# Kernel optimization log

Hardware: AMD Instinct MI355X
Metric: run time of the kernel (lower is better)

The kernel has to match this reference:

```python
import jax, jax.numpy as jnp
import numpy as np

FP8_MAX = 448.0  # float8_e4m3 max finite value


def setup_inputs() -> dict:
    key = jax.random.key(0)
    k1, k2, k3, k4, k5 = jax.random.split(key, 5)
    B, S, IN, OUT = 8, 2048, 2048, 2048
    x = jax.random.normal(k1, (B, S, IN), dtype=jnp.float32)
    weight = jax.random.normal(k2, (OUT, IN), dtype=jnp.float32) * 0.02
    bias = jax.random.normal(k3, (OUT,), dtype=jnp.float32)
    # per-tensor scales, kept positive and away from zero
    scale_in = jax.random.uniform(k4, (1,), dtype=jnp.float32) * 0.09 + 0.01
    scale_w = jax.random.uniform(k5, (1,), dtype=jnp.float32) * 0.09 + 0.01
    return {"x": x, "weight": weight, "bias": bias,
            "scale_in": scale_in, "scale_w": scale_w}


def _fp8_quantize(x, scale):
    # divide by scale, saturate to fp8 range, cast to fp8 e4m3
    q = jnp.clip(x / scale, -FP8_MAX, FP8_MAX)
    return q.astype(jnp.float8_e4m3fn)


def reference(x, weight, bias, scale_in, scale_w):
    # quantize input and weight to fp8 (per-tensor scales)
    xq = _fp8_quantize(x, scale_in)            # [B,S,IN] fp8
    wq = _fp8_quantize(weight, scale_w)        # [OUT,IN] fp8
    # scaled matmul: accumulate in fp32, dequant with scale_a*scale_b, emit fp16
    acc = jnp.einsum('bsk,nk->bsn', xq.astype(jnp.float32), wq.astype(jnp.float32))
    out = (acc * (scale_in[0] * scale_w[0])).astype(jnp.float16)
    out = out + bias.astype(jnp.float16)       # trailing bias add at fp16
    return out
```

## Files before the change

kernel.cpp:

```cpp
#include <hip/hip_runtime.h>
#include <hip/hip_fp16.h>
#include <stdint.h>

#define MDIM 16384
#define NDIM 2048
#define KDIM 2048

typedef __attribute__((ext_vector_type(4))) float f32x4;
typedef __attribute__((ext_vector_type(4))) int   i32x4;
typedef __attribute__((ext_vector_type(8))) int   i32x8;

__device__ __forceinline__ unsigned f32_to_e4m3(float x) {
    float q = fminf(448.f, fmaxf(-448.f, x));
    unsigned ub = __float_as_uint(q);
    unsigned sgn = (ub >> 24) & 0x80u;
    float aq = fabsf(q);
    int E = (int)((__float_as_uint(aq) >> 23) & 0xff) - 127;
    if (E < -6) E = -6;
    float rq = __uint_as_float((unsigned)(130 - E) << 23);
    int m = (int)rintf(aq * rq);
    if (m == 16) { m = 8; E += 1; }
    unsigned bits;
    if (m < 8) bits = sgn | (unsigned)m;
    else       bits = sgn | ((unsigned)(E + 7) << 3) | (unsigned)(m - 8);
    return bits;
}

__device__ __forceinline__ void quant_span(const float* __restrict__ x,
                                           uint8_t* __restrict__ q, float sc,
                                           unsigned i0, unsigned stride,
                                           unsigned n16) {
    for (unsigned i = i0; i < n16; i += stride) {
        const float4* xp = (const float4*)(x + (size_t)i * 16);
        uint32_t w[4];
#pragma unroll
        for (int j = 0; j < 4; ++j) {
            float4 v = xp[j];
            w[j] = f32_to_e4m3(v.x / sc) | (f32_to_e4m3(v.y / sc) << 8) |
                   (f32_to_e4m3(v.z / sc) << 16) | (f32_to_e4m3(v.w / sc) << 24);
        }
        ((uint4*)q)[i] = make_uint4(w[0], w[1], w[2], w[3]);
    }
}

__global__ void quant_both_kernel(const float* __restrict__ x,
                                  uint8_t* __restrict__ xq,
                                  const float* __restrict__ w,
                                  uint8_t* __restrict__ wq,
                                  const float* __restrict__ s_in,
                                  const float* __restrict__ s_w) {
    if (blockIdx.x < 2048) {
        unsigned i0 = blockIdx.x * 256 + threadIdx.x;
        quant_span(x, xq, s_in[0], i0, 2048 * 256,
                   (unsigned)((size_t)MDIM * KDIM / 16));
    } else {
        unsigned i0 = (blockIdx.x - 2048) * 256 + threadIdx.x;
        quant_span(w, wq, s_w[0], i0, 256 * 256,
                   (unsigned)((size_t)NDIM * KDIM / 16));
    }
}

#define BM 256
#define BN 256
#define BKB 128
#define NKT (KDIM / BKB)

__device__ __forceinline__ void gload_lds16(const uint8_t* g, uint8_t* l) {
    __builtin_amdgcn_global_load_lds(
        (const __attribute__((address_space(1))) void*)g,
        (__attribute__((address_space(3))) void*)l, 16, 0, 0);
}

__device__ __forceinline__ void barrier_raw() {
    asm volatile("" ::: "memory");
    __builtin_amdgcn_s_barrier();
    asm volatile("" ::: "memory");
}

__global__ __launch_bounds__(512) void gemm_fp8_kernel(
    const uint8_t* __restrict__ Aq, const uint8_t* __restrict__ Bq,
    const float* __restrict__ bias, const float* __restrict__ s_in,
    const float* __restrict__ s_w, float* __restrict__ out) {

    extern __shared__ uint8_t lds[];

    int nwg = gridDim.x;
    int cpx = nwg >> 3;
    int bid = blockIdx.x;
    int swz = (bid & 7) * cpx + (bid >> 3);
    int tm = swz >> 3;
    int tn = swz & 7;
    int row0 = tm * BM;
    int col0 = tn * BN;

    int tid  = threadIdx.x;
    int lane = tid & 63;
    int wid  = tid >> 6;
    int wr = wid >> 2, wc = wid & 3;
    int r15 = lane & 15;
    int g   = lane >> 4;

    int perm0 = ((2 * g + r15) & 7) << 4;
    int perm1 = ((2 * g + 1 + r15) & 7) << 4;

    int up0 = tid, up1 = 512 + tid;
    int ur0 = up0 >> 3, uc0 = ((up0 & 7) - (ur0 & 7)) & 7;
    int ur1 = up1 >> 3, uc1 = ((up1 & 7) - (ur1 & 7)) & 7;

    const uint8_t* Asrc = Aq + (size_t)row0 * KDIM;
    const uint8_t* Bsrc = Bq + (size_t)col0 * KDIM;

#define STAGE_U(MAT, H, KT)                                                   \
    {                                                                         \
        uint8_t* dst_ = &lds[(((unsigned)(KT) & 1) << 16) + (MAT) * 32768 +   \
                             (H) * 16384];                                    \
        const uint8_t* src_ = (MAT) ? Bsrc : Asrc;                            \
        gload_lds16(src_ + (size_t)((H) * 128 + ur0) * KDIM +                 \
                        (size_t)(KT) * BKB + uc0 * 16,                        \
                    dst_ + up0 * 16);                                         \
        gload_lds16(src_ + (size_t)((H) * 128 + ur1) * KDIM +                 \
                        (size_t)(KT) * BKB + uc1 * 16,                        \
                    dst_ + up1 * 16);                                         \
    }

    f32x4 acc[8][4];
#pragma unroll
    for (int m = 0; m < 8; ++m)
#pragma unroll
        for (int n = 0; n < 4; ++n)
            acc[m][n] = (f32x4){0.f, 0.f, 0.f, 0.f};

    i32x8 af[4], bf[4];

    int aRow0 = wr * 128 + r15;
    int bRow0 = (wc >> 1) * 128 + (wc & 1) * 64 + r15;

#define LOAD_AF(bo, MH)                                                       \
    _Pragma("unroll")                                                         \
    for (int m_ = 0; m_ < 4; ++m_) {                                          \
        const uint8_t* rp = lds + (bo) + (aRow0 + (MH) * 64 + m_ * 16) * 128; \
        i32x4 lo = *(const i32x4*)(rp + perm0);                               \
        i32x4 hi = *(const i32x4*)(rp + perm1);                               \
        _Pragma("unroll")                                                     \
        for (int q_ = 0; q_ < 4; ++q_) { af[m_][q_] = lo[q_]; af[m_][4 + q_] = hi[q_]; } \
    }

#define LOAD_BF2(bo, NH)                                                      \
    _Pragma("unroll")                                                         \
    for (int n_ = 2 * (NH); n_ < 2 * (NH) + 2; ++n_) {                        \
        const uint8_t* rp = lds + (bo) + 32768 + (bRow0 + n_ * 16) * 128;     \
        i32x4 lo = *(const i32x4*)(rp + perm0);                               \
        i32x4 hi = *(const i32x4*)(rp + perm1);                               \
        _Pragma("unroll")                                                     \
        for (int q_ = 0; q_ < 4; ++q_) { bf[n_][q_] = lo[q_]; bf[n_][4 + q_] = hi[q_]; } \
    }

#define MFMA8(MH, NH)                                                         \
    __builtin_amdgcn_s_setprio(1);                                            \
    _Pragma("unroll")                                                         \
    for (int m_ = 0; m_ < 4; ++m_)                                            \
        _Pragma("unroll")                                                     \
        for (int n_ = 2 * (NH); n_ < 2 * (NH) + 2; ++n_)                      \
            acc[(MH) * 4 + m_][n_] =                                          \
                __builtin_amdgcn_mfma_scale_f32_16x16x128_f8f6f4(             \
                    af[m_], bf[n_], acc[(MH) * 4 + m_][n_],                   \
                    0, 0, 0, 127, 0, 127);                                    \
    __builtin_amdgcn_s_setprio(0);

#define LGKM0 asm volatile("s_waitcnt lgkmcnt(0)" ::: "memory")

    STAGE_U(0, 0, 0); STAGE_U(0, 1, 0); STAGE_U(1, 0, 0); STAGE_U(1, 1, 0);
    STAGE_U(1, 0, 1); STAGE_U(1, 1, 1);
    asm volatile("s_waitcnt vmcnt(4)" ::: "memory");
    barrier_raw();

    for (int t = 0; t < NKT; ++t) {
        const unsigned bo = (unsigned)(t & 1) << 16;
        LOAD_AF(bo, 0);
        LOAD_BF2(bo, 0);
        if (t + 1 < NKT) STAGE_U(0, 0, t + 1);
        barrier_raw(); LGKM0;
        MFMA8(0, 0);
        barrier_raw();
        LOAD_BF2(bo, 1);
        if (t + 1 < NKT) STAGE_U(0, 1, t + 1);
        barrier_raw(); LGKM0;
        MFMA8(0, 1);
        barrier_raw();
        LOAD_AF(bo, 1);
        if (t + 2 < NKT) STAGE_U(1, 0, t + 2);
        barrier_raw(); LGKM0;
        MFMA8(1, 0);
        barrier_raw();
        if (t + 2 < NKT) STAGE_U(1, 1, t + 2);
        barrier_raw(); LGKM0;
        MFMA8(1, 1);
        if (t + 2 < NKT) asm volatile("s_waitcnt vmcnt(4)" ::: "memory");
        else             asm volatile("s_waitcnt vmcnt(0)" ::: "memory");
        barrier_raw();
    }

    float s = s_in[0] * s_w[0];
    float* slab = (float*)lds;
    __half hb[4];
#pragma unroll
    for (int n = 0; n < 4; ++n)
        hb[n] = __float2half(bias[col0 + wc * 64 + n * 16 + r15]);

#pragma unroll
    for (int mh = 0; mh < 2; ++mh) {
#pragma unroll
        for (int n = 0; n < 4; ++n) {
            int colb = wc * 64 + n * 16 + r15;
#pragma unroll
            for (int m = 0; m < 4; ++m) {
                int sr = wr * 64 + m * 16 + g * 4;
#pragma unroll
                for (int r = 0; r < 4; ++r) {
                    __half h = __float2half(acc[mh * 4 + m][n][r] * s);
                    slab[(sr + r) * 256 + colb] = __half2float(__hadd(h, hb[n]));
                }
            }
        }
        barrier_raw();
#pragma unroll
        for (int it = 0; it < 16; ++it) {
            int srow = wid * 16 + it;
            f32x4 vv = *(const f32x4*)&slab[srow * 256 + lane * 4];
            int grow = row0 + (srow >> 6) * 128 + mh * 64 + (srow & 63);
            *(f32x4*)&out[(size_t)grow * NDIM + col0 + lane * 4] = vv;
        }
        barrier_raw();
    }
#undef STAGE_U
#undef LOAD_AF
#undef LOAD_BF2
#undef MFMA8
#undef LGKM0
}

extern "C" void kernel_launch(void* const* d_in, const int* in_sizes, int n_in,
                              void* d_out, int out_size, void* d_ws, size_t ws_size,
                              hipStream_t stream) {
    const float* x      = (const float*)d_in[0];
    const float* weight = (const float*)d_in[1];
    const float* bias   = (const float*)d_in[2];
    const float* s_in   = (const float*)d_in[3];
    const float* s_w    = (const float*)d_in[4];
    float* out          = (float*)d_out;

    uint8_t* xq = (uint8_t*)d_ws;
    uint8_t* wq = (uint8_t*)d_ws + (size_t)MDIM * KDIM;

    quant_both_kernel<<<2304, 256, 0, stream>>>(x, xq, weight, wq, s_in, s_w);

    dim3 grid((MDIM / BM) * (NDIM / BN));
    gemm_fp8_kernel<<<grid, 512, 131072, stream>>>(xq, wq, bias, s_in, s_w, out);
}
```

Baseline: 126.9 us.

## Use 4 waves with 128x128 per-wave tiles and simplified double-buffered K loop

```diff
diff --git a/kernel.cpp b/kernel.cpp
--- a/kernel.cpp
+++ b/kernel.cpp
@@ -77,7 +77,7 @@
     asm volatile("" ::: "memory");
 }
 
-__global__ __launch_bounds__(512) void gemm_fp8_kernel(
+__global__ __launch_bounds__(256, 1) void gemm_fp8_kernel(
     const uint8_t* __restrict__ Aq, const uint8_t* __restrict__ Bq,
     const float* __restrict__ bias, const float* __restrict__ s_in,
     const float* __restrict__ s_w, float* __restrict__ out) {
@@ -96,129 +96,120 @@
     int tid  = threadIdx.x;
     int lane = tid & 63;
     int wid  = tid >> 6;
-    int wr = wid >> 2, wc = wid & 3;
+    int wr = wid >> 1, wc = wid & 1;
     int r15 = lane & 15;
     int g   = lane >> 4;
 
     int perm0 = ((2 * g + r15) & 7) << 4;
     int perm1 = ((2 * g + 1 + r15) & 7) << 4;
 
-    int up0 = tid, up1 = 512 + tid;
-    int ur0 = up0 >> 3, uc0 = ((up0 & 7) - (ur0 & 7)) & 7;
-    int ur1 = up1 >> 3, uc1 = ((up1 & 7) - (ur1 & 7)) & 7;
-
+    int stoff[8], sdst[8];
+#pragma unroll
+    for (int j = 0; j < 8; ++j) {
+        int p = j * 256 + tid;
+        int row = p >> 3;
+        int c = ((p & 7) - (row & 7)) & 7;
+        stoff[j] = row * KDIM + c * 16;
+        sdst[j]  = p * 16;
+    }
     const uint8_t* Asrc = Aq + (size_t)row0 * KDIM;
     const uint8_t* Bsrc = Bq + (size_t)col0 * KDIM;
 
-#define STAGE_U(MAT, H, KT)                                                   \
+#define STAGE(KT)                                                             \
     {                                                                         \
-        uint8_t* dst_ = &lds[(((unsigned)(KT) & 1) << 16) + (MAT) * 32768 +   \
-                             (H) * 16384];                                    \
-        const uint8_t* src_ = (MAT) ? Bsrc : Asrc;                            \
-        gload_lds16(src_ + (size_t)((H) * 128 + ur0) * KDIM +                 \
-                        (size_t)(KT) * BKB + uc0 * 16,                        \
-                    dst_ + up0 * 16);                                         \
-        gload_lds16(src_ + (size_t)((H) * 128 + ur1) * KDIM +                 \
-                        (size_t)(KT) * BKB + uc1 * 16,                        \
-                    dst_ + up1 * 16);                                         \
-    }
-
-    f32x4 acc[8][4];
+        uint8_t* dst_ = &lds[((unsigned)(KT) & 1) << 16];                     \
+        _Pragma("unroll")                                                     \
+        for (int j_ = 0; j_ < 8; ++j_)                                        \
+            gload_lds16(Asrc + stoff[j_] + (size_t)(KT) * BKB, dst_ + sdst[j_]); \
+        _Pragma("unroll")                                                     \
+        for (int j_ = 0; j_ < 8; ++j_)                                        \
+            gload_lds16(Bsrc + stoff[j_] + (size_t)(KT) * BKB,                \
+                        dst_ + 32768 + sdst[j_]);                             \
+    }
+
+    f32x4 acc[8][8];
 #pragma unroll
     for (int m = 0; m < 8; ++m)
 #pragma unroll
-        for (int n = 0; n < 4; ++n)
+        for (int n = 0; n < 8; ++n)
             acc[m][n] = (f32x4){0.f, 0.f, 0.f, 0.f};
 
-    i32x8 af[4], bf[4];
-
+    i32x8 af[8], bf0, bf1;
     int aRow0 = wr * 128 + r15;
-    int bRow0 = (wc >> 1) * 128 + (wc & 1) * 64 + r15;
-
-#define LOAD_AF(bo, MH)                                                       \
+    int bRow0 = wc * 128 + r15;
+
+#define LOAD_AF(bo)                                                           \
     _Pragma("unroll")                                                         \
-    for (int m_ = 0; m_ < 4; ++m_) {                                          \
-        const uint8_t* rp = lds + (bo) + (aRow0 + (MH) * 64 + m_ * 16) * 128; \
+    for (int m_ = 0; m_ < 8; ++m_) {                                          \
+        const uint8_t* rp = lds + (bo) + (aRow0 + m_ * 16) * 128;             \
         i32x4 lo = *(const i32x4*)(rp + perm0);                               \
         i32x4 hi = *(const i32x4*)(rp + perm1);                               \
         _Pragma("unroll")                                                     \
         for (int q_ = 0; q_ < 4; ++q_) { af[m_][q_] = lo[q_]; af[m_][4 + q_] = hi[q_]; } \
     }
 
-#define LOAD_BF2(bo, NH)                                                      \
-    _Pragma("unroll")                                                         \
-    for (int n_ = 2 * (NH); n_ < 2 * (NH) + 2; ++n_) {                        \
-        const uint8_t* rp = lds + (bo) + 32768 + (bRow0 + n_ * 16) * 128;     \
+#define LDBF(DST, bo, N)                                                      \
+    {                                                                         \
+        const uint8_t* rp = lds + (bo) + 32768 + (bRow0 + (N) * 16) * 128;    \
         i32x4 lo = *(const i32x4*)(rp + perm0);                               \
         i32x4 hi = *(const i32x4*)(rp + perm1);                               \
         _Pragma("unroll")                                                     \
-        for (int q_ = 0; q_ < 4; ++q_) { bf[n_][q_] = lo[q_]; bf[n_][4 + q_] = hi[q_]; } \
-    }
-
-#define MFMA8(MH, NH)                                                         \
+        for (int q_ = 0; q_ < 4; ++q_) { DST[q_] = lo[q_]; DST[4 + q_] = hi[q_]; } \
+    }
+
+#define MFMA_COL(BF, N)                                                       \
     __builtin_amdgcn_s_setprio(1);                                            \
     _Pragma("unroll")                                                         \
-    for (int m_ = 0; m_ < 4; ++m_)                                            \
-        _Pragma("unroll")                                                     \
-        for (int n_ = 2 * (NH); n_ < 2 * (NH) + 2; ++n_)                      \
-            acc[(MH) * 4 + m_][n_] =                                          \
-                __builtin_amdgcn_mfma_scale_f32_16x16x128_f8f6f4(             \
-                    af[m_], bf[n_], acc[(MH) * 4 + m_][n_],                   \
-                    0, 0, 0, 127, 0, 127);                                    \
+    for (int m_ = 0; m_ < 8; ++m_)                                            \
+        acc[m_][N] = __builtin_amdgcn_mfma_scale_f32_16x16x128_f8f6f4(        \
+            af[m_], BF, acc[m_][N], 0, 0, 0, 127, 0, 127);                    \
     __builtin_amdgcn_s_setprio(0);
 
-#define LGKM0 asm volatile("s_waitcnt lgkmcnt(0)" ::: "memory")
-
-    STAGE_U(0, 0, 0); STAGE_U(0, 1, 0); STAGE_U(1, 0, 0); STAGE_U(1, 1, 0);
-    STAGE_U(1, 0, 1); STAGE_U(1, 1, 1);
-    asm volatile("s_waitcnt vmcnt(4)" ::: "memory");
-    barrier_raw();
+    STAGE(0);
+    STAGE(1);
 
     for (int t = 0; t < NKT; ++t) {
+        if (t + 1 < NKT) asm volatile("s_waitcnt vmcnt(16)" ::: "memory");
+        else             asm volatile("s_waitcnt vmcnt(0)" ::: "memory");
+        barrier_raw();
         const unsigned bo = (unsigned)(t & 1) << 16;
-        LOAD_AF(bo, 0);
-        LOAD_BF2(bo, 0);
-        if (t + 1 < NKT) STAGE_U(0, 0, t + 1);
-        barrier_raw(); LGKM0;
-        MFMA8(0, 0);
-        barrier_raw();
-        LOAD_BF2(bo, 1);
-        if (t + 1 < NKT) STAGE_U(0, 1, t + 1);
-        barrier_raw(); LGKM0;
-        MFMA8(0, 1);
-        barrier_raw();
-        LOAD_AF(bo, 1);
-        if (t + 2 < NKT) STAGE_U(1, 0, t + 2);
-        barrier_raw(); LGKM0;
-        MFMA8(1, 0);
-        barrier_raw();
-        if (t + 2 < NKT) STAGE_U(1, 1, t + 2);
-        barrier_raw(); LGKM0;
-        MFMA8(1, 1);
-        if (t + 2 < NKT) asm volatile("s_waitcnt vmcnt(4)" ::: "memory");
-        else             asm volatile("s_waitcnt vmcnt(0)" ::: "memory");
-        barrier_raw();
+        LOAD_AF(bo);
+        LDBF(bf0, bo, 0);
+        LDBF(bf1, bo, 1); MFMA_COL(bf0, 0);
+        LDBF(bf0, bo, 2); MFMA_COL(bf1, 1);
+        LDBF(bf1, bo, 3); MFMA_COL(bf0, 2);
+        LDBF(bf0, bo, 4); MFMA_COL(bf1, 3);
+        LDBF(bf1, bo, 5); MFMA_COL(bf0, 4);
+        LDBF(bf0, bo, 6); MFMA_COL(bf1, 5);
+        LDBF(bf1, bo, 7); MFMA_COL(bf0, 6);
+                          MFMA_COL(bf1, 7);
+        barrier_raw();
+        if (t + 2 < NKT) STAGE(t + 2);
     }
 
     float s = s_in[0] * s_w[0];
     float* slab = (float*)lds;
-    __half hb[4];
-#pragma unroll
-    for (int n = 0; n < 4; ++n)
-        hb[n] = __float2half(bias[col0 + wc * 64 + n * 16 + r15]);
-
-#pragma unroll
-    for (int mh = 0; mh < 2; ++mh) {
-#pragma unroll
-        for (int n = 0; n < 4; ++n) {
-            int colb = wc * 64 + n * 16 + r15;
-#pragma unroll
-            for (int m = 0; m < 4; ++m) {
-                int sr = wr * 64 + m * 16 + g * 4;
-#pragma unroll
-                for (int r = 0; r < 4; ++r) {
-                    __half h = __float2half(acc[mh * 4 + m][n][r] * s);
-                    slab[(sr + r) * 256 + colb] = __half2float(__hadd(h, hb[n]));
+    __half hb[8];
+#pragma unroll
+    for (int n = 0; n < 8; ++n)
+        hb[n] = __float2half(bias[col0 + wc * 128 + n * 16 + r15]);
+
+#pragma unroll
+    for (int q = 0; q < 4; ++q) {
+        if (wr == (q >> 1)) {
+            const int mh = q & 1;
+#pragma unroll
+            for (int n = 0; n < 8; ++n) {
+                int colb = wc * 128 + n * 16 + r15;
+#pragma unroll
+                for (int m = 0; m < 4; ++m) {
+                    int sr = m * 16 + g * 4;
+#pragma unroll
+                    for (int r = 0; r < 4; ++r) {
+                        __half h = __float2half(acc[mh * 4 + m][n][r] * s);
+                        slab[(sr + r) * 256 + colb] =
+                            __half2float(__hadd(h, hb[n]));
+                    }
                 }
             }
         }
@@ -227,16 +218,15 @@
         for (int it = 0; it < 16; ++it) {
             int srow = wid * 16 + it;
             f32x4 vv = *(const f32x4*)&slab[srow * 256 + lane * 4];
-            int grow = row0 + (srow >> 6) * 128 + mh * 64 + (srow & 63);
+            int grow = row0 + q * 64 + srow;
             *(f32x4*)&out[(size_t)grow * NDIM + col0 + lane * 4] = vv;
         }
         barrier_raw();
     }
-#undef STAGE_U
+#undef STAGE
 #undef LOAD_AF
-#undef LOAD_BF2
-#undef MFMA8
-#undef LGKM0
+#undef LDBF
+#undef MFMA_COL
 }
 
 extern "C" void kernel_launch(void* const* d_in, const int* in_sizes, int n_in,
@@ -255,5 +245,5 @@
     quant_both_kernel<<<2304, 256, 0, stream>>>(x, xq, weight, wq, s_in, s_w);
 
     dim3 grid((MDIM / BM) * (NDIM / BN));
-    gemm_fp8_kernel<<<grid, 512, 131072, stream>>>(xq, wq, bias, s_in, s_w, out);
-}
+    gemm_fp8_kernel<<<grid, 256, 131072, stream>>>(xq, wq, bias, s_in, s_w, out);
+}
```

After: 127.4 us. About the same (+0.4%).
